# Performance work log

Measured on AMD Instinct MI355X. Metric: run time of the kernel, lower is better.

Reference implementation:

```python
import jax, jax.numpy as jnp
import numpy as np

N = 4096
D = 256          # hidden_dim
H = 8            # num_heads
HD = D // H      # head_dim
EPS = 1e-5
SCALE = D ** -0.5  # note: full hidden_dim, as in the torch code


def setup_inputs() -> dict:
    key = jax.random.key(0)
    ks = jax.random.split(key, 12)
    # binary-ish adjacency mask in [0,1); zeros/near-zeros act like masked entries
    A = (jax.random.uniform(ks[0], (N, N)) < 0.01).astype(jnp.float32)
    h = jax.random.normal(ks[1], (N, D), dtype=jnp.float32)
    s = D ** -0.5
    Wq = jax.random.normal(ks[2], (D, D), dtype=jnp.float32) * s
    Wk = jax.random.normal(ks[3], (D, D), dtype=jnp.float32) * s
    Wv = jax.random.normal(ks[4], (D, D), dtype=jnp.float32) * s
    Wo = jax.random.normal(ks[5], (D, D), dtype=jnp.float32) * s
    g1 = jnp.ones((D,), jnp.float32)
    b1 = jnp.zeros((D,), jnp.float32)
    g2 = jnp.ones((D,), jnp.float32)
    b2 = jnp.zeros((D,), jnp.float32)
    W1 = jax.random.normal(ks[6], (2 * D, D), dtype=jnp.float32) * s
    W2 = jax.random.normal(ks[7], (D, 2 * D), dtype=jnp.float32) * (2 * D) ** -0.5
    return {"A": A, "h": h, "Wq": Wq, "Wk": Wk, "Wv": Wv, "Wo": Wo,
            "g1": g1, "b1": b1, "g2": g2, "b2": b2, "W1": W1, "W2": W2}


def _batchnorm(x, g, b):
    # training-mode BatchNorm1d over node/batch dim, biased variance
    m = x.mean(axis=0)
    v = x.var(axis=0)
    return (x - m) * jax.lax.rsqrt(v + EPS) * g + b


def _mha(A, h, Wq, Wk, Wv, Wo):
    # torch reshape(N, head_dim, num_heads): head index is the fastest axis
    q = (h @ Wq.T).reshape(N, HD, H) * SCALE   # [N, hd, H]
    k = (h @ Wk.T).reshape(N, HD, H)
    v = (h @ Wv.T).reshape(N, HD, H)
    scores = jnp.einsum('ndh,mdh->hnm', q, k)  # [H, N, N]
    attn = jax.nn.softmax(A[None, :, :] * scores, axis=2)
    out = jnp.einsum('hnm,mdh->ndh', attn, v)  # [N, hd, H]
    return out.reshape(N, D) @ Wo.T


def reference(A, h, Wq, Wk, Wv, Wo, g1, b1, g2, b2, W1, W2):
    h1 = h
    h = _mha(A, h, Wq, Wk, Wv, Wo)
    h = h + h1                       # residual
    h = _batchnorm(h, g1, b1)
    h2 = h
    h = jax.nn.relu(h @ W1.T) @ W2.T  # FFN (no bias)
    h = h2 + h                       # residual
    h = _batchnorm(h, g2, b2)
    return h
```

## Files before the change

kernel.cpp:

```cpp
#include <hip/hip_runtime.h>
#include <math.h>

#define NN 4096
#define DIM 256
#define NHEAD 8
#define HDIM 32
#define DFF 512
#define CAP 128
#define EPS_BN 1e-5f
#define QSCALE 0.0625f
#define MB (1u << 20)

typedef __attribute__((ext_vector_type(8))) short short8;
typedef __attribute__((ext_vector_type(4))) float f32x4;

__device__ inline ushort f2bf(float x) {
    unsigned u = __builtin_bit_cast(unsigned, x);
    unsigned r = u + 0x7FFF + ((u >> 16) & 1);
    return (ushort)(r >> 16);
}
__device__ inline float bf2f(ushort u) {
    return __builtin_bit_cast(float, (unsigned)u << 16);
}
__device__ inline float bflo(unsigned u) { return __builtin_bit_cast(float, u << 16); }
__device__ inline float bfhi(unsigned u) { return __builtin_bit_cast(float, u & 0xFFFF0000u); }

__global__ __launch_bounds__(256) void convert_bf(
    const float* __restrict__ s0, const float* __restrict__ s1,
    const float* __restrict__ s2, const float* __restrict__ s3,
    const float* __restrict__ s4, const float* __restrict__ s5,
    const float* __restrict__ s6,
    ushort* d0, ushort* d1, ushort* d2, ushort* d3,
    ushort* d4, ushort* d5, ushort* d6)
{
    int b = blockIdx.x, tid = threadIdx.x;
    if (b >= 608 && b < 640) {
        int off = b - 608;
        int row = off * 8 + (tid >> 5), t = tid & 31;
        int hh = t >> 2, dd0 = (t & 3) * 8;
        const float* src = s4 + (size_t)row * 256 + hh;
        ushort tmp[8];
        #pragma unroll
        for (int i = 0; i < 8; ++i) tmp[i] = f2bf(src[(size_t)(dd0 + i) * 8]);
        uint4 u;
        u.x = (unsigned)tmp[0] | ((unsigned)tmp[1] << 16);
        u.y = (unsigned)tmp[2] | ((unsigned)tmp[3] << 16);
        u.z = (unsigned)tmp[4] | ((unsigned)tmp[5] << 16);
        u.w = (unsigned)tmp[6] | ((unsigned)tmp[7] << 16);
        *(uint4*)(d4 + (size_t)row * 256 + hh * 32 + dd0) = u;
        return;
    }
    const float* s; ushort* d; int off;
    if      (b < 512) { s = s0; d = d0; off = b; }
    else if (b < 544) { s = s1; d = d1; off = b - 512; }
    else if (b < 576) { s = s2; d = d2; off = b - 544; }
    else if (b < 608) { s = s3; d = d3; off = b - 576; }
    else if (b < 704) { s = s5; d = d5; off = b - 640; }
    else              { s = s6; d = d6; off = b - 704; }
    size_t base = (size_t)off * 2048 + (size_t)tid * 8;
    float4 f0 = *(const float4*)(s + base);
    float4 f1 = *(const float4*)(s + base + 4);
    uint4 u;
    u.x = (unsigned)f2bf(f0.x) | ((unsigned)f2bf(f0.y) << 16);
    u.y = (unsigned)f2bf(f0.z) | ((unsigned)f2bf(f0.w) << 16);
    u.z = (unsigned)f2bf(f1.x) | ((unsigned)f2bf(f1.y) << 16);
    u.w = (unsigned)f2bf(f1.z) | ((unsigned)f2bf(f1.w) << 16);
    *(uint4*)(d + base) = u;
}

#define LDP 88
#define TSTRIDE 74
__global__ __launch_bounds__(256) void qkv_ascan(
    const ushort* __restrict__ Ah, const ushort* __restrict__ B,
    ushort* __restrict__ qh, ushort* __restrict__ kvh,
    float* __restrict__ vpart,
    const float* __restrict__ Araw, unsigned* __restrict__ packed,
    int* __restrict__ cnt)
{
    __shared__ ushort As[64][LDP];
    __shared__ ushort Bs[64][LDP];
    __shared__ float sRedS[8][64];
    int b = blockIdx.x, tid = threadIdx.x;

    if (b >= 768) {
        int* scan = (int*)&As[0][0];
        int n = b - 768;
        const float* row = Araw + (size_t)n * NN;
        float4 vals[4];
        int c = 0;
        #pragma unroll
        for (int i = 0; i < 4; ++i) {
            vals[i] = *(const float4*)(row + i * 1024 + tid * 4);
            c += (vals[i].x != 0.f) + (vals[i].y != 0.f)
               + (vals[i].z != 0.f) + (vals[i].w != 0.f);
        }
        scan[tid] = c;
        __syncthreads();
        for (int off = 1; off < 256; off <<= 1) {
            int t = (tid >= off) ? scan[tid - off] : 0;
            __syncthreads();
            scan[tid] += t;
            __syncthreads();
        }
        int pos = scan[tid] - c;
        int total = scan[255];
        #pragma unroll
        for (int i = 0; i < 4; ++i) {
            int cb = i * 1024 + tid * 4;
            float4 v = vals[i];
            if (v.x != 0.f && pos < CAP) { packed[n*CAP+pos] = ((unsigned)f2bf(v.x) << 16) | (unsigned)cb;       ++pos; }
            if (v.y != 0.f && pos < CAP) { packed[n*CAP+pos] = ((unsigned)f2bf(v.y) << 16) | (unsigned)(cb + 1); ++pos; }
            if (v.z != 0.f && pos < CAP) { packed[n*CAP+pos] = ((unsigned)f2bf(v.z) << 16) | (unsigned)(cb + 2); ++pos; }
            if (v.w != 0.f && pos < CAP) { packed[n*CAP+pos] = ((unsigned)f2bf(v.w) << 16) | (unsigned)(cb + 3); ++pos; }
        }
        if (tid == 0) cnt[n] = min(total, CAP);
        return;
    }

    int lane = tid & 63, w = tid >> 6;
    int wm = (w >> 1) * 32, wn = (w & 1) * 32;
    int xcd = b & 7, pos = b >> 3;
    int by = xcd * 8 + pos / 12;
    int bx = pos % 12;
    int m0 = by * 64, n0 = bx * 64;
    int l15 = lane & 15, lk = lane >> 4;
    int srow = tid >> 3;
    int scol = (tid & 7) * 8;

    f32x4 acc[2][2] = {};
    for (int k0 = 0; k0 < DIM; k0 += 64) {
        const ushort* Bg = B + (size_t)(n0 + srow) * DIM + scol + k0;
        uint4 gb0 = *(const uint4*)Bg;
        uint4 gb1 = *(const uint4*)(Bg + (size_t)32 * DIM);
        const ushort* Ag = Ah + (size_t)(m0 + srow) * DIM + scol + k0;
        uint4 ga0 = *(const uint4*)Ag;
        uint4 ga1 = *(const uint4*)(Ag + (size_t)32 * DIM);
        __syncthreads();
        *(uint4*)&As[srow][scol]      = ga0;
        *(uint4*)&As[srow + 32][scol] = ga1;
        *(uint4*)&Bs[srow][scol]      = gb0;
        *(uint4*)&Bs[srow + 32][scol] = gb1;
        __syncthreads();
        #pragma unroll
        for (int ks = 0; ks < 2; ++ks) {
            int kc = ks * 32 + lk * 8;
            short8 a0 = *(const short8*)&As[wm      + l15][kc];
            short8 a1 = *(const short8*)&As[wm + 16 + l15][kc];
            short8 b0 = *(const short8*)&Bs[wn      + l15][kc];
            short8 b1 = *(const short8*)&Bs[wn + 16 + l15][kc];
            acc[0][0] = __builtin_amdgcn_mfma_f32_16x16x32_bf16(a0, b0, acc[0][0], 0, 0, 0);
            acc[0][1] = __builtin_amdgcn_mfma_f32_16x16x32_bf16(a0, b1, acc[0][1], 0, 0, 0);
            acc[1][0] = __builtin_amdgcn_mfma_f32_16x16x32_bf16(a1, b0, acc[1][0], 0, 0, 0);
            acc[1][1] = __builtin_amdgcn_mfma_f32_16x16x32_bf16(a1, b1, acc[1][1], 0, 0, 0);
        }
    }
    ushort* sT = &As[0][0];
    int seg = n0 >> 8, ddBase = (n0 & 255) >> 3;
    float sp[2] = {0.f, 0.f};
    __syncthreads();
    #pragma unroll
    for (int mt = 0; mt < 2; ++mt)
        #pragma unroll
        for (int nt = 0; nt < 2; ++nt) {
            int col_l = wn + nt * 16 + l15;
            #pragma unroll
            for (int i = 0; i < 4; ++i) {
                int row_l = wm + mt * 16 + lk * 4 + i;
                float v = acc[mt][nt][i];
                if (seg == 0) v *= QSCALE;
                sT[row_l * TSTRIDE + col_l] = f2bf(v);
                sp[nt] += v;
            }
        }
    __syncthreads();
    for (int c = tid; c < 512; c += 256) {
        int rl = c & 63, hh = c >> 6;
        const ushort* tp = sT + rl * TSTRIDE + hh;
        uint4 pk;
        pk.x = (unsigned)tp[0]  | ((unsigned)tp[8]  << 16);
        pk.y = (unsigned)tp[16] | ((unsigned)tp[24] << 16);
        pk.z = (unsigned)tp[32] | ((unsigned)tp[40] << 16);
        pk.w = (unsigned)tp[48] | ((unsigned)tp[56] << 16);
        int row = m0 + rl;
        if (seg == 0)
            *(uint4*)(qh + ((size_t)hh * NN + row) * HDIM + ddBase) = pk;
        else
            *(uint4*)(kvh + ((size_t)hh * NN + row) * 64 +
                      ((seg == 2) ? 32 : 0) + ddBase) = pk;
    }
    if (seg == 2) {
        int slot = ((wm >> 5) << 2) | lk;
        sRedS[slot][wn + l15]      = sp[0];
        sRedS[slot][wn + 16 + l15] = sp[1];
        __syncthreads();
        if (tid < 64) {
            float ss = 0.f;
            #pragma unroll
            for (int r = 0; r < 8; ++r) ss += sRedS[r][tid];
            vpart[(size_t)by * 256 + (n0 & 255) + tid] = ss;
        }
    }
}

__global__ __launch_bounds__(256) void gemm_bf(
    const void* __restrict__ Aptr, const ushort* __restrict__ B,
    const float* __restrict__ scA, const float* __restrict__ shA,
    const float* __restrict__ resid,
    const float* yres, const float* __restrict__ scR, const float* __restrict__ shR,
    float* Cf, ushort* __restrict__ Cb,
    float* __restrict__ bnps, float* __restrict__ bnpq,
    int M, int Nn, int K, int aMode, int storeMode, int relu, int bnstat)
{
    __shared__ ushort As[64][LDP];
    __shared__ ushort Bs[64][LDP];
    __shared__ float sRedS[8][64];
    __shared__ float sRedQ[8][64];
    int tid = threadIdx.x;
    int lane = tid & 63, w = tid >> 6;
    int wm = (w >> 1) * 32, wn = (w & 1) * 32;
    int nbx = gridDim.x, nbyq = gridDim.y >> 3;
    int orig = blockIdx.y * nbx + blockIdx.x;
    int xcd = orig & 7, pos = orig >> 3;
    int by = xcd * nbyq + pos / nbx;
    int bx = pos % nbx;
    int m0 = by * 64, n0 = bx * 64;
    int l15 = lane & 15, lk = lane >> 4;
    int srow = tid >> 3;
    int scol = (tid & 7) * 8;

    f32x4 acc[2][2] = {};
    for (int k0 = 0; k0 < K; k0 += 64) {
        uint4 ga0, ga1, gb0, gb1;
        const ushort* Bg = B + (size_t)(n0 + srow) * K + scol + k0;
        gb0 = *(const uint4*)Bg;
        gb1 = *(const uint4*)(Bg + (size_t)32 * K);
        if (aMode == 0) {
            const ushort* Ag = (const ushort*)Aptr + (size_t)(m0 + srow) * K + scol + k0;
            ga0 = *(const uint4*)Ag;
            ga1 = *(const uint4*)(Ag + (size_t)32 * K);
        } else if (aMode == 2) {
            int c0 = k0 + scol;
            int hh = c0 >> 5, dd = c0 & 31;
            const ushort* Ag = (const ushort*)Aptr +
                ((size_t)hh * NN + m0 + srow) * HDIM + dd;
            ga0 = *(const uint4*)Ag;
            ga1 = *(const uint4*)(Ag + (size_t)32 * HDIM);
        } else {
            const float* Af = (const float*)Aptr + (size_t)(m0 + srow) * K + scol + k0;
            float4 sc0 = *(const float4*)(scA + k0 + scol);
            float4 sc1 = *(const float4*)(scA + k0 + scol + 4);
            float4 sh0 = *(const float4*)(shA + k0 + scol);
            float4 sh1 = *(const float4*)(shA + k0 + scol + 4);
            float4 a0 = *(const float4*)Af;
            float4 a1 = *(const float4*)(Af + 4);
            float4 b0 = *(const float4*)(Af + (size_t)32 * K);
            float4 b1 = *(const float4*)(Af + (size_t)32 * K + 4);
            ga0.x = (unsigned)f2bf(a0.x*sc0.x+sh0.x) | ((unsigned)f2bf(a0.y*sc0.y+sh0.y) << 16);
            ga0.y = (unsigned)f2bf(a0.z*sc0.z+sh0.z) | ((unsigned)f2bf(a0.w*sc0.w+sh0.w) << 16);
            ga0.z = (unsigned)f2bf(a1.x*sc1.x+sh1.x) | ((unsigned)f2bf(a1.y*sc1.y+sh1.y) << 16);
            ga0.w = (unsigned)f2bf(a1.z*sc1.z+sh1.z) | ((unsigned)f2bf(a1.w*sc1.w+sh1.w) << 16);
            ga1.x = (unsigned)f2bf(b0.x*sc0.x+sh0.x) | ((unsigned)f2bf(b0.y*sc0.y+sh0.y) << 16);
            ga1.y = (unsigned)f2bf(b0.z*sc0.z+sh0.z) | ((unsigned)f2bf(b0.w*sc0.w+sh0.w) << 16);
            ga1.z = (unsigned)f2bf(b1.x*sc1.x+sh1.x) | ((unsigned)f2bf(b1.y*sc1.y+sh1.y) << 16);
            ga1.w = (unsigned)f2bf(b1.z*sc1.z+sh1.z) | ((unsigned)f2bf(b1.w*sc1.w+sh1.w) << 16);
        }
        __syncthreads();
        *(uint4*)&As[srow][scol]      = ga0;
        *(uint4*)&As[srow + 32][scol] = ga1;
        *(uint4*)&Bs[srow][scol]      = gb0;
        *(uint4*)&Bs[srow + 32][scol] = gb1;
        __syncthreads();
        #pragma unroll
        for (int ks = 0; ks < 2; ++ks) {
            int kc = ks * 32 + lk * 8;
            short8 a0 = *(const short8*)&As[wm      + l15][kc];
            short8 a1 = *(const short8*)&As[wm + 16 + l15][kc];
            short8 b0 = *(const short8*)&Bs[wn      + l15][kc];
            short8 b1 = *(const short8*)&Bs[wn + 16 + l15][kc];
            acc[0][0] = __builtin_amdgcn_mfma_f32_16x16x32_bf16(a0, b0, acc[0][0], 0, 0, 0);
            acc[0][1] = __builtin_amdgcn_mfma_f32_16x16x32_bf16(a0, b1, acc[0][1], 0, 0, 0);
            acc[1][0] = __builtin_amdgcn_mfma_f32_16x16x32_bf16(a1, b0, acc[1][0], 0, 0, 0);
            acc[1][1] = __builtin_amdgcn_mfma_f32_16x16x32_bf16(a1, b1, acc[1][1], 0, 0, 0);
        }
    }

    float sp[2] = {0.f, 0.f}, qp[2] = {0.f, 0.f};
    #pragma unroll
    for (int mt = 0; mt < 2; ++mt) {
        #pragma unroll
        for (int nt = 0; nt < 2; ++nt) {
            int col = n0 + wn + nt * 16 + l15;
            #pragma unroll
            for (int i = 0; i < 4; ++i) {
                int row = m0 + wm + mt * 16 + lk * 4 + i;
                float v = acc[mt][nt][i];
                if (storeMode == 0) {
                    if (resid) v += resid[(size_t)row * Nn + col];
                    Cf[(size_t)row * Nn + col] = v;
                } else if (storeMode == 1) {
                    if (relu) v = fmaxf(v, 0.f);
                    Cb[(size_t)row * Nn + col] = f2bf(v);
                } else {
                    v += yres[(size_t)row * Nn + col] * scR[col] + shR[col];
                    Cf[(size_t)row * Nn + col] = v;
                }
                if (bnstat) { sp[nt] += v; qp[nt] += v * v; }
            }
        }
    }
    if (bnstat) {
        int slot = ((wm >> 5) << 2) | lk;
        sRedS[slot][wn + l15]      = sp[0];
        sRedQ[slot][wn + l15]      = qp[0];
        sRedS[slot][wn + 16 + l15] = sp[1];
        sRedQ[slot][wn + 16 + l15] = qp[1];
        __syncthreads();
        if (tid < 64) {
            float ss = 0.f, qq = 0.f;
            #pragma unroll
            for (int r = 0; r < 8; ++r) { ss += sRedS[r][tid]; qq += sRedQ[r][tid]; }
            bnps[(size_t)by * DIM + n0 + tid] = ss;
            bnpq[(size_t)by * DIM + n0 + tid] = qq;
        }
    }
}

__global__ __launch_bounds__(256) void vsum_final(
    const float* __restrict__ vpart, float* __restrict__ vsumh)
{
    int c = threadIdx.x;
    float s = 0.f;
    #pragma unroll 8
    for (int b = 0; b < 64; ++b) s += vpart[(size_t)b * 256 + c];
    vsumh[(c & 7) * HDIM + (c >> 3)] = s;
}

__global__ __launch_bounds__(1024) void colreduce_final2(
    const float* __restrict__ ps, const float* __restrict__ pq,
    const float* __restrict__ g, const float* __restrict__ bsh,
    float* __restrict__ scale, float* __restrict__ shift)
{
    __shared__ float rs_[4][256], rq_[4][256];
    int t = threadIdx.x;
    int c = t & 255, qd = t >> 8;
    float s = 0.f, q = 0.f;
    for (int b = qd; b < 64; b += 4) {
        s += ps[b * DIM + c];
        q += pq[b * DIM + c];
    }
    rs_[qd][c] = s; rq_[qd][c] = q;
    __syncthreads();
    if (qd == 0) {
        s = rs_[0][c] + rs_[1][c] + rs_[2][c] + rs_[3][c];
        q = rq_[0][c] + rq_[1][c] + rq_[2][c] + rq_[3][c];
        float m = s * (1.f / NN);
        float var = q * (1.f / NN) - m * m;
        float rstd = rsqrtf(var + EPS_BN);
        float sc = rstd * g[c];
        scale[c] = sc;
        shift[c] = bsh[c] - m * sc;
    }
}

__global__ __launch_bounds__(256) void bn_apply_fin(
    const float* __restrict__ x, const float* __restrict__ scale,
    const float* __restrict__ shift, float* __restrict__ out)
{
    int tid = threadIdx.x;
    size_t i = (size_t)blockIdx.x * 1024 + (size_t)tid * 4;
    int c = (tid * 4) & 255;
    float4 v = *(const float4*)(x + i);
    float4 sc = *(const float4*)(scale + c);
    float4 sh = *(const float4*)(shift + c);
    float4 r;
    r.x = v.x * sc.x + sh.x;
    r.y = v.y * sc.y + sh.y;
    r.z = v.z * sc.z + sh.z;
    r.w = v.w * sc.w + sh.w;
    *(float4*)(out + i) = r;
}

__global__ __launch_bounds__(256) void attn3(
    const ushort* __restrict__ qh, const ushort* __restrict__ kvh,
    const float* __restrict__ vsumh,
    const unsigned* __restrict__ packed, const int* __restrict__ cnt,
    ushort* __restrict__ outh)
{
    __shared__ float    sQ[8][32];
    __shared__ unsigned sPk[8][CAP];
    __shared__ float    sS[8][CAP];
    __shared__ float    sRd[8];

    int tid = threadIdx.x, b = blockIdx.x;
    int hH = b & 7, rg = b >> 3;
    int r = tid >> 5, l = tid & 31;
    int n = rg * 8 + r;
    int nnz = cnt[n];

    sQ[r][l] = bf2f(qh[((size_t)hH * NN + n) * HDIM + l]);
    for (int j = l; j < nnz; j += 32) sPk[r][j] = packed[n * CAP + j];
    __syncthreads();

    float4 qreg[8];
    #pragma unroll
    for (int t = 0; t < 8; ++t) qreg[t] = ((const float4*)sQ[r])[t];
    float lsum = 0.0f;
    for (int j = l; j < nnz; j += 32) {
        unsigned pk = sPk[r][j];
        int m = pk & 0xFFFF;
        float a = bfhi(pk);
        const uint4* kp = (const uint4*)(kvh + ((size_t)hH * NN + m) * 64);
        uint4 k0 = kp[0], k1 = kp[1], k2 = kp[2], k3 = kp[3];
        float s =
            bflo(k0.x)*qreg[0].x + bfhi(k0.x)*qreg[0].y +
            bflo(k0.y)*qreg[0].z + bfhi(k0.y)*qreg[0].w +
            bflo(k0.z)*qreg[1].x + bfhi(k0.z)*qreg[1].y +
            bflo(k0.w)*qreg[1].z + bfhi(k0.w)*qreg[1].w +
            bflo(k1.x)*qreg[2].x + bfhi(k1.x)*qreg[2].y +
            bflo(k1.y)*qreg[2].z + bfhi(k1.y)*qreg[2].w +
            bflo(k1.z)*qreg[3].x + bfhi(k1.z)*qreg[3].y +
            bflo(k1.w)*qreg[3].z + bfhi(k1.w)*qreg[3].w +
            bflo(k2.x)*qreg[4].x + bfhi(k2.x)*qreg[4].y +
            bflo(k2.y)*qreg[4].z + bfhi(k2.y)*qreg[4].w +
            bflo(k2.z)*qreg[5].x + bfhi(k2.z)*qreg[5].y +
            bflo(k2.w)*qreg[5].z + bfhi(k2.w)*qreg[5].w +
            bflo(k3.x)*qreg[6].x + bfhi(k3.x)*qreg[6].y +
            bflo(k3.y)*qreg[6].z + bfhi(k3.y)*qreg[6].w +
            bflo(k3.z)*qreg[7].x + bfhi(k3.z)*qreg[7].y +
            bflo(k3.w)*qreg[7].z + bfhi(k3.w)*qreg[7].w;
        s *= a;
        float ww = __expf(s);
        sS[r][j] = ww - 1.0f;
        lsum += ww;
    }
    #pragma unroll
    for (int o = 16; o > 0; o >>= 1) lsum += __shfl_xor(lsum, o, 32);
    if (l == 0) sRd[r] = 1.0f / (lsum + (float)(NN - nnz));
    __syncthreads();

    int jsub = l >> 3, dq = l & 7;
    const ushort* vbase = kvh + (size_t)hH * NN * 64 + 32 + dq * 4;
    float a0 = 0.f, a1 = 0.f, a2 = 0.f, a3 = 0.f;
    for (int j = jsub; j < nnz; j += 4) {
        float ww = sS[r][j];
        int m = sPk[r][j] & 0xFFFF;
        uint2 vv = *(const uint2*)(vbase + (size_t)m * 64);
        a0 += ww * bflo(vv.x); a1 += ww * bfhi(vv.x);
        a2 += ww * bflo(vv.y); a3 += ww * bfhi(vv.y);
    }
    #pragma unroll
    for (int o = 8; o < 32; o <<= 1) {
        a0 += __shfl_xor(a0, o, 32);
        a1 += __shfl_xor(a1, o, 32);
        a2 += __shfl_xor(a2, o, 32);
        a3 += __shfl_xor(a3, o, 32);
    }
    if (jsub == 0) {
        float rd = sRd[r];
        int d0 = dq * 4;
        const float* vs = vsumh + hH * HDIM + d0;
        float r0 = (a0 + vs[0]) * rd;
        float r1 = (a1 + vs[1]) * rd;
        float r2 = (a2 + vs[2]) * rd;
        float r3 = (a3 + vs[3]) * rd;
        uint2 st;
        st.x = (unsigned)f2bf(r0) | ((unsigned)f2bf(r1) << 16);
        st.y = (unsigned)f2bf(r2) | ((unsigned)f2bf(r3) << 16);
        *(uint2*)(outh + ((size_t)hH * NN + n) * HDIM + d0) = st;
    }
}

extern "C" void kernel_launch(void* const* d_in, const int* in_sizes, int n_in,
                              void* d_out, int out_size, void* d_ws, size_t ws_size,
                              hipStream_t stream)
{
    const float* A  = (const float*)d_in[0];
    const float* h  = (const float*)d_in[1];
    const float* Wq = (const float*)d_in[2];
    const float* Wk = (const float*)d_in[3];
    const float* Wv = (const float*)d_in[4];
    const float* Wo = (const float*)d_in[5];
    const float* g1 = (const float*)d_in[6];
    const float* b1 = (const float*)d_in[7];
    const float* g2 = (const float*)d_in[8];
    const float* b2 = (const float*)d_in[9];
    const float* W1 = (const float*)d_in[10];
    const float* W2 = (const float*)d_in[11];
    float* out = (float*)d_out;
    char* w = (char*)d_ws;

    unsigned* packed = (unsigned*)(w);
    int*    nzcnt  = (int*)(w + 2 * MB);
    ushort* h_bf   = (ushort*)(w + 3 * MB);
    ushort* wqkv   = (ushort*)(w + 5 * MB);
    ushort* wo_b   = (ushort*)(w + 5 * MB + 384 * 1024);
    ushort* w1_b   = (ushort*)(w + 5 * MB + 512 * 1024);
    ushort* w2_b   = (ushort*)(w + 5 * MB + 768 * 1024);
    ushort* qh_bf  = (ushort*)(w + 6 * MB);
    ushort* kvh    = (ushort*)(w + 8 * MB);
    ushort* ao_hb  = (ushort*)(w + 12 * MB);
    float*  y      = (float*)(w + 14 * MB);
    ushort* t_bf   = (ushort*)(w + 18 * MB);
    float*  vpart  = (float*)(w + 22 * MB);
    float*  bnps   = (float*)(w + 23 * MB);
    float*  bnpq   = (float*)(w + 23 * MB + 64 * 1024);
    float*  scale1 = (float*)(w + 24 * MB);
    float*  shift1 = scale1 + 256;
    float*  scale2 = scale1 + 512;
    float*  shift2 = scale1 + 768;
    float*  vsumh  = scale1 + 1024;

    dim3 blk(256);

    convert_bf<<<768, blk, 0, stream>>>(h, Wq, Wk, Wv, Wo, W1, W2,
        h_bf, wqkv, wqkv + 65536, wqkv + 131072, wo_b, w1_b, w2_b);
    qkv_ascan<<<4864, blk, 0, stream>>>(h_bf, wqkv, qh_bf, kvh, vpart,
                                        A, packed, nzcnt);
    vsum_final<<<1, blk, 0, stream>>>(vpart, vsumh);
    attn3<<<NN, blk, 0, stream>>>(qh_bf, kvh, vsumh, packed, nzcnt, ao_hb);
    gemm_bf<<<dim3(4, 64), blk, 0, stream>>>(ao_hb, wo_b,
        nullptr, nullptr, h, nullptr, nullptr, nullptr,
        y, nullptr, bnps, bnpq, NN, DIM, DIM, 2, 0, 0, 1);
    colreduce_final2<<<1, dim3(1024), 0, stream>>>(bnps, bnpq, g1, b1, scale1, shift1);
    gemm_bf<<<dim3(8, 64), blk, 0, stream>>>(y, w1_b,
        scale1, shift1, nullptr, nullptr, nullptr, nullptr,
        nullptr, t_bf, nullptr, nullptr, NN, DFF, DIM, 1, 1, 1, 0);
    gemm_bf<<<dim3(4, 64), blk, 0, stream>>>(t_bf, w2_b,
        nullptr, nullptr, nullptr, y, scale1, shift1,
        y, nullptr, bnps, bnpq, NN, DIM, DFF, 0, 3, 0, 1);
    colreduce_final2<<<1, dim3(1024), 0, stream>>>(bnps, bnpq, g2, b2, scale2, shift2);
    bn_apply_fin<<<1024, blk, 0, stream>>>(y, scale2, shift2, out);
}
```

Before: 94.94 us.

## Fold reduction finalizers into producer kernels via last-block atomics; convert h inline

Removes the separate vsum_final and colreduce_final2 launches by having the last-finishing block (detected with an atomic counter and threadfence) do the final column reduction inside qkv_ascan and the BN-stat gemm_bf calls. The fp32 input h is now converted to bf16 while being loaded into the QKV GEMM instead of in a separate pass, so convert_w handles only the weights and resets the counters. This cuts three kernel launches and one global round trip for h_bf. In exchange, each GEMM tile now converts its A operand itself, and one block per kernel does a serial 64-row reduction at the tail.

```diff
diff --git a/kernel.cpp b/kernel.cpp
--- a/kernel.cpp
+++ b/kernel.cpp
@@ -25,20 +25,21 @@
 __device__ inline float bflo(unsigned u) { return __builtin_bit_cast(float, u << 16); }
 __device__ inline float bfhi(unsigned u) { return __builtin_bit_cast(float, u & 0xFFFF0000u); }
 
-__global__ __launch_bounds__(256) void convert_bf(
-    const float* __restrict__ s0, const float* __restrict__ s1,
-    const float* __restrict__ s2, const float* __restrict__ s3,
-    const float* __restrict__ s4, const float* __restrict__ s5,
-    const float* __restrict__ s6,
-    ushort* d0, ushort* d1, ushort* d2, ushort* d3,
-    ushort* d4, ushort* d5, ushort* d6)
+__global__ __launch_bounds__(256) void convert_w(
+    const float* __restrict__ Wq, const float* __restrict__ Wk,
+    const float* __restrict__ Wv, const float* __restrict__ Wo,
+    const float* __restrict__ W1, const float* __restrict__ W2,
+    ushort* __restrict__ wqkv, ushort* __restrict__ wo_b,
+    ushort* __restrict__ w1_b, ushort* __restrict__ w2_b,
+    int* __restrict__ cnts)
 {
     int b = blockIdx.x, tid = threadIdx.x;
-    if (b >= 608 && b < 640) {
-        int off = b - 608;
+    if (b == 0 && tid < 8) cnts[tid] = 0;
+    if (b >= 96 && b < 128) {
+        int off = b - 96;
         int row = off * 8 + (tid >> 5), t = tid & 31;
         int hh = t >> 2, dd0 = (t & 3) * 8;
-        const float* src = s4 + (size_t)row * 256 + hh;
+        const float* src = Wo + (size_t)row * 256 + hh;
         ushort tmp[8];
         #pragma unroll
         for (int i = 0; i < 8; ++i) tmp[i] = f2bf(src[(size_t)(dd0 + i) * 8]);
@@ -47,16 +48,15 @@
         u.y = (unsigned)tmp[2] | ((unsigned)tmp[3] << 16);
         u.z = (unsigned)tmp[4] | ((unsigned)tmp[5] << 16);
         u.w = (unsigned)tmp[6] | ((unsigned)tmp[7] << 16);
-        *(uint4*)(d4 + (size_t)row * 256 + hh * 32 + dd0) = u;
+        *(uint4*)(wo_b + (size_t)row * 256 + hh * 32 + dd0) = u;
         return;
     }
     const float* s; ushort* d; int off;
-    if      (b < 512) { s = s0; d = d0; off = b; }
-    else if (b < 544) { s = s1; d = d1; off = b - 512; }
-    else if (b < 576) { s = s2; d = d2; off = b - 544; }
-    else if (b < 608) { s = s3; d = d3; off = b - 576; }
-    else if (b < 704) { s = s5; d = d5; off = b - 640; }
-    else              { s = s6; d = d6; off = b - 704; }
+    if      (b < 32)  { s = Wq; d = wqkv;          off = b; }
+    else if (b < 64)  { s = Wk; d = wqkv + 65536;  off = b - 32; }
+    else if (b < 96)  { s = Wv; d = wqkv + 131072; off = b - 64; }
+    else if (b < 192) { s = W1; d = w1_b;          off = b - 128; }
+    else              { s = W2; d = w2_b;          off = b - 192; }
     size_t base = (size_t)off * 2048 + (size_t)tid * 8;
     float4 f0 = *(const float4*)(s + base);
     float4 f1 = *(const float4*)(s + base + 4);
@@ -71,15 +71,16 @@
 #define LDP 88
 #define TSTRIDE 74
 __global__ __launch_bounds__(256) void qkv_ascan(
-    const ushort* __restrict__ Ah, const ushort* __restrict__ B,
+    const float* __restrict__ hF, const ushort* __restrict__ B,
     ushort* __restrict__ qh, ushort* __restrict__ kvh,
-    float* __restrict__ vpart,
+    float* __restrict__ vpart, float* __restrict__ vsumh,
     const float* __restrict__ Araw, unsigned* __restrict__ packed,
-    int* __restrict__ cnt)
+    int* __restrict__ cnt, int* __restrict__ cntV)
 {
     __shared__ ushort As[64][LDP];
     __shared__ ushort Bs[64][LDP];
     __shared__ float sRedS[8][64];
+    __shared__ int lastF;
     int b = blockIdx.x, tid = threadIdx.x;
 
     if (b >= 768) {
@@ -132,9 +133,20 @@
         const ushort* Bg = B + (size_t)(n0 + srow) * DIM + scol + k0;
         uint4 gb0 = *(const uint4*)Bg;
         uint4 gb1 = *(const uint4*)(Bg + (size_t)32 * DIM);
-        const ushort* Ag = Ah + (size_t)(m0 + srow) * DIM + scol + k0;
-        uint4 ga0 = *(const uint4*)Ag;
-        uint4 ga1 = *(const uint4*)(Ag + (size_t)32 * DIM);
+        const float* Af = hF + (size_t)(m0 + srow) * DIM + scol + k0;
+        float4 a0 = *(const float4*)Af;
+        float4 a1 = *(const float4*)(Af + 4);
+        float4 c0 = *(const float4*)(Af + (size_t)32 * DIM);
+        float4 c1 = *(const float4*)(Af + (size_t)32 * DIM + 4);
+        uint4 ga0, ga1;
+        ga0.x = (unsigned)f2bf(a0.x) | ((unsigned)f2bf(a0.y) << 16);
+        ga0.y = (unsigned)f2bf(a0.z) | ((unsigned)f2bf(a0.w) << 16);
+        ga0.z = (unsigned)f2bf(a1.x) | ((unsigned)f2bf(a1.y) << 16);
+        ga0.w = (unsigned)f2bf(a1.z) | ((unsigned)f2bf(a1.w) << 16);
+        ga1.x = (unsigned)f2bf(c0.x) | ((unsigned)f2bf(c0.y) << 16);
+        ga1.y = (unsigned)f2bf(c0.z) | ((unsigned)f2bf(c0.w) << 16);
+        ga1.z = (unsigned)f2bf(c1.x) | ((unsigned)f2bf(c1.y) << 16);
+        ga1.w = (unsigned)f2bf(c1.z) | ((unsigned)f2bf(c1.w) << 16);
         __syncthreads();
         *(uint4*)&As[srow][scol]      = ga0;
         *(uint4*)&As[srow + 32][scol] = ga1;
@@ -144,14 +156,14 @@
         #pragma unroll
         for (int ks = 0; ks < 2; ++ks) {
             int kc = ks * 32 + lk * 8;
-            short8 a0 = *(const short8*)&As[wm      + l15][kc];
-            short8 a1 = *(const short8*)&As[wm + 16 + l15][kc];
-            short8 b0 = *(const short8*)&Bs[wn      + l15][kc];
-            short8 b1 = *(const short8*)&Bs[wn + 16 + l15][kc];
-            acc[0][0] = __builtin_amdgcn_mfma_f32_16x16x32_bf16(a0, b0, acc[0][0], 0, 0, 0);
-            acc[0][1] = __builtin_amdgcn_mfma_f32_16x16x32_bf16(a0, b1, acc[0][1], 0, 0, 0);
-            acc[1][0] = __builtin_amdgcn_mfma_f32_16x16x32_bf16(a1, b0, acc[1][0], 0, 0, 0);
-            acc[1][1] = __builtin_amdgcn_mfma_f32_16x16x32_bf16(a1, b1, acc[1][1], 0, 0, 0);
+            short8 a0s = *(const short8*)&As[wm      + l15][kc];
+            short8 a1s = *(const short8*)&As[wm + 16 + l15][kc];
+            short8 b0s = *(const short8*)&Bs[wn      + l15][kc];
+            short8 b1s = *(const short8*)&Bs[wn + 16 + l15][kc];
+            acc[0][0] = __builtin_amdgcn_mfma_f32_16x16x32_bf16(a0s, b0s, acc[0][0], 0, 0, 0);
+            acc[0][1] = __builtin_amdgcn_mfma_f32_16x16x32_bf16(a0s, b1s, acc[0][1], 0, 0, 0);
+            acc[1][0] = __builtin_amdgcn_mfma_f32_16x16x32_bf16(a1s, b0s, acc[1][0], 0, 0, 0);
+            acc[1][1] = __builtin_amdgcn_mfma_f32_16x16x32_bf16(a1s, b1s, acc[1][1], 0, 0, 0);
         }
     }
     ushort* sT = &As[0][0];
@@ -199,6 +211,17 @@
             for (int r = 0; r < 8; ++r) ss += sRedS[r][tid];
             vpart[(size_t)by * 256 + (n0 & 255) + tid] = ss;
         }
+        __threadfence();
+        if (tid == 0) lastF = (atomicAdd(cntV, 1) == 255);
+        __syncthreads();
+        if (lastF) {
+            __threadfence();
+            int c = tid;
+            float s = 0.f;
+            #pragma unroll 8
+            for (int bb = 0; bb < 64; ++bb) s += vpart[(size_t)bb * 256 + c];
+            vsumh[(c & 7) * HDIM + (c >> 3)] = s;
+        }
     }
 }
 
@@ -209,12 +232,16 @@
     const float* yres, const float* __restrict__ scR, const float* __restrict__ shR,
     float* Cf, ushort* __restrict__ Cb,
     float* __restrict__ bnps, float* __restrict__ bnpq,
+    int* __restrict__ lastCnt, const float* __restrict__ g,
+    const float* __restrict__ bsh, float* __restrict__ scaleOut,
+    float* __restrict__ shiftOut,
     int M, int Nn, int K, int aMode, int storeMode, int relu, int bnstat)
 {
     __shared__ ushort As[64][LDP];
     __shared__ ushort Bs[64][LDP];
     __shared__ float sRedS[8][64];
     __shared__ float sRedQ[8][64];
+    __shared__ int lastF;
     int tid = threadIdx.x;
     int lane = tid & 63, w = tid >> 6;
     int wm = (w >> 1) * 32, wn = (w & 1) * 32;
@@ -322,43 +349,26 @@
             bnps[(size_t)by * DIM + n0 + tid] = ss;
             bnpq[(size_t)by * DIM + n0 + tid] = qq;
         }
-    }
-}
-
-__global__ __launch_bounds__(256) void vsum_final(
-    const float* __restrict__ vpart, float* __restrict__ vsumh)
-{
-    int c = threadIdx.x;
-    float s = 0.f;
-    #pragma unroll 8
-    for (int b = 0; b < 64; ++b) s += vpart[(size_t)b * 256 + c];
-    vsumh[(c & 7) * HDIM + (c >> 3)] = s;
-}
-
-__global__ __launch_bounds__(1024) void colreduce_final2(
-    const float* __restrict__ ps, const float* __restrict__ pq,
-    const float* __restrict__ g, const float* __restrict__ bsh,
-    float* __restrict__ scale, float* __restrict__ shift)
-{
-    __shared__ float rs_[4][256], rq_[4][256];
-    int t = threadIdx.x;
-    int c = t & 255, qd = t >> 8;
-    float s = 0.f, q = 0.f;
-    for (int b = qd; b < 64; b += 4) {
-        s += ps[b * DIM + c];
-        q += pq[b * DIM + c];
-    }
-    rs_[qd][c] = s; rq_[qd][c] = q;
-    __syncthreads();
-    if (qd == 0) {
-        s = rs_[0][c] + rs_[1][c] + rs_[2][c] + rs_[3][c];
-        q = rq_[0][c] + rq_[1][c] + rq_[2][c] + rq_[3][c];
-        float m = s * (1.f / NN);
-        float var = q * (1.f / NN) - m * m;
-        float rstd = rsqrtf(var + EPS_BN);
-        float sc = rstd * g[c];
-        scale[c] = sc;
-        shift[c] = bsh[c] - m * sc;
+        __threadfence();
+        if (tid == 0)
+            lastF = (atomicAdd(lastCnt, 1) == (int)(gridDim.x * gridDim.y) - 1);
+        __syncthreads();
+        if (lastF) {
+            __threadfence();
+            int c = tid;
+            float s = 0.f, q = 0.f;
+            #pragma unroll 4
+            for (int bb = 0; bb < 64; ++bb) {
+                s += bnps[(size_t)bb * DIM + c];
+                q += bnpq[(size_t)bb * DIM + c];
+            }
+            float m = s * (1.f / NN);
+            float var = q * (1.f / NN) - m * m;
+            float rstd = rsqrtf(var + EPS_BN);
+            float sc = rstd * g[c];
+            scaleOut[c] = sc;
+            shiftOut[c] = bsh[c] - m * sc;
+        }
     }
 }
 
@@ -491,7 +501,6 @@
 
     unsigned* packed = (unsigned*)(w);
     int*    nzcnt  = (int*)(w + 2 * MB);
-    ushort* h_bf   = (ushort*)(w + 3 * MB);
     ushort* wqkv   = (ushort*)(w + 5 * MB);
     ushort* wo_b   = (ushort*)(w + 5 * MB + 384 * 1024);
     ushort* w1_b   = (ushort*)(w + 5 * MB + 512 * 1024);
@@ -502,32 +511,35 @@
     float*  y      = (float*)(w + 14 * MB);
     ushort* t_bf   = (ushort*)(w + 18 * MB);
     float*  vpart  = (float*)(w + 22 * MB);
-    float*  bnps   = (float*)(w + 23 * MB);
-    float*  bnpq   = (float*)(w + 23 * MB + 64 * 1024);
+    float*  bnps1  = (float*)(w + 23 * MB);
+    float*  bnpq1  = (float*)(w + 23 * MB + 64 * 1024);
+    float*  bnps2  = (float*)(w + 23 * MB + 128 * 1024);
+    float*  bnpq2  = (float*)(w + 23 * MB + 192 * 1024);
     float*  scale1 = (float*)(w + 24 * MB);
     float*  shift1 = scale1 + 256;
     float*  scale2 = scale1 + 512;
     float*  shift2 = scale1 + 768;
     float*  vsumh  = scale1 + 1024;
+    int*    cnts   = (int*)(w + 25 * MB);
 
     dim3 blk(256);
 
-    convert_bf<<<768, blk, 0, stream>>>(h, Wq, Wk, Wv, Wo, W1, W2,
-        h_bf, wqkv, wqkv + 65536, wqkv + 131072, wo_b, w1_b, w2_b);
-    qkv_ascan<<<4864, blk, 0, stream>>>(h_bf, wqkv, qh_bf, kvh, vpart,
-                                        A, packed, nzcnt);
-    vsum_final<<<1, blk, 0, stream>>>(vpart, vsumh);
+    convert_w<<<256, blk, 0, stream>>>(Wq, Wk, Wv, Wo, W1, W2,
+        wqkv, wo_b, w1_b, w2_b, cnts);
+    qkv_ascan<<<4864, blk, 0, stream>>>(h, wqkv, qh_bf, kvh, vpart, vsumh,
+                                        A, packed, nzcnt, cnts + 0);
     attn3<<<NN, blk, 0, stream>>>(qh_bf, kvh, vsumh, packed, nzcnt, ao_hb);
     gemm_bf<<<dim3(4, 64), blk, 0, stream>>>(ao_hb, wo_b,
         nullptr, nullptr, h, nullptr, nullptr, nullptr,
-        y, nullptr, bnps, bnpq, NN, DIM, DIM, 2, 0, 0, 1);
-    colreduce_final2<<<1, dim3(1024), 0, stream>>>(bnps, bnpq, g1, b1, scale1, shift1);
+        y, nullptr, bnps1, bnpq1, cnts + 1, g1, b1, scale1, shift1,
+        NN, DIM, DIM, 2, 0, 0, 1);
     gemm_bf<<<dim3(8, 64), blk, 0, stream>>>(y, w1_b,
         scale1, shift1, nullptr, nullptr, nullptr, nullptr,
-        nullptr, t_bf, nullptr, nullptr, NN, DFF, DIM, 1, 1, 1, 0);
+        nullptr, t_bf, nullptr, nullptr, nullptr, nullptr, nullptr,
+        nullptr, nullptr, NN, DFF, DIM, 1, 1, 1, 0);
     gemm_bf<<<dim3(4, 64), blk, 0, stream>>>(t_bf, w2_b,
         nullptr, nullptr, nullptr, y, scale1, shift1,
-        y, nullptr, bnps, bnpq, NN, DIM, DFF, 0, 3, 0, 1);
-    colreduce_final2<<<1, dim3(1024), 0, stream>>>(bnps, bnpq, g2, b2, scale2, shift2);
+        y, nullptr, bnps2, bnpq2, cnts + 2, g2, b2, scale2, shift2,
+        NN, DIM, DFF, 0, 3, 0, 1);
     bn_apply_fin<<<1024, blk, 0, stream>>>(y, scale2, shift2, out);
 }
```

Measured after the change: 164.1 us. 1.73x slower.

## Fuse attention score and value accumulation into one pass per neighbor

Applied to the files above, without the earlier changes.

The sparse attention kernel now loads K and V for each neighbor in the same pass and accumulates exp-weighted V into 32 per-lane registers. This replaces the separate second loop that re-gathered V rows and read scores back from shared memory. A transposed shared-memory reduction across lanes then produces the output, in two batches to bound LDS use. The cost is higher register pressure (32 accumulators) and a larger LDS reduction with extra barriers. Q is also kept packed as bf16 and unpacked on the fly.

```diff
diff --git a/kernel.cpp b/kernel.cpp
--- a/kernel.cpp
+++ b/kernel.cpp
@@ -200,6 +200,16 @@
             vpart[(size_t)by * 256 + (n0 & 255) + tid] = ss;
         }
     }
+}
+
+__global__ __launch_bounds__(256) void vsum_final(
+    const float* __restrict__ vpart, float* __restrict__ vsumh)
+{
+    int c = threadIdx.x;
+    float s = 0.f;
+    #pragma unroll 8
+    for (int b = 0; b < 64; ++b) s += vpart[(size_t)b * 256 + c];
+    vsumh[(c & 7) * HDIM + (c >> 3)] = s;
 }
 
 __global__ __launch_bounds__(256) void gemm_bf(
@@ -325,16 +335,6 @@
     }
 }
 
-__global__ __launch_bounds__(256) void vsum_final(
-    const float* __restrict__ vpart, float* __restrict__ vsumh)
-{
-    int c = threadIdx.x;
-    float s = 0.f;
-    #pragma unroll 8
-    for (int b = 0; b < 64; ++b) s += vpart[(size_t)b * 256 + c];
-    vsumh[(c & 7) * HDIM + (c >> 3)] = s;
-}
-
 __global__ __launch_bounds__(1024) void colreduce_final2(
     const float* __restrict__ ps, const float* __restrict__ pq,
     const float* __restrict__ g, const float* __restrict__ bsh,
@@ -380,16 +380,16 @@
     *(float4*)(out + i) = r;
 }
 
-__global__ __launch_bounds__(256) void attn3(
+__global__ __launch_bounds__(256) void attn4(
     const ushort* __restrict__ qh, const ushort* __restrict__ kvh,
     const float* __restrict__ vsumh,
     const unsigned* __restrict__ packed, const int* __restrict__ cnt,
     ushort* __restrict__ outh)
 {
-    __shared__ float    sQ[8][32];
+    __shared__ unsigned sQp[8][16];
     __shared__ unsigned sPk[8][CAP];
-    __shared__ float    sS[8][CAP];
     __shared__ float    sRd[8];
+    __shared__ float    sRed[4][32][33];
 
     int tid = threadIdx.x, b = blockIdx.x;
     int hH = b & 7, rg = b >> 3;
@@ -397,76 +397,82 @@
     int n = rg * 8 + r;
     int nnz = cnt[n];
 
-    sQ[r][l] = bf2f(qh[((size_t)hH * NN + n) * HDIM + l]);
+    if (l < 16)
+        sQp[r][l] = ((const unsigned*)(qh + ((size_t)hH * NN + n) * HDIM))[l];
     for (int j = l; j < nnz; j += 32) sPk[r][j] = packed[n * CAP + j];
     __syncthreads();
 
-    float4 qreg[8];
+    float acc[32];
     #pragma unroll
-    for (int t = 0; t < 8; ++t) qreg[t] = ((const float4*)sQ[r])[t];
-    float lsum = 0.0f;
+    for (int i = 0; i < 32; ++i) acc[i] = 0.f;
+    float lsum = 0.f;
+
     for (int j = l; j < nnz; j += 32) {
         unsigned pk = sPk[r][j];
         int m = pk & 0xFFFF;
         float a = bfhi(pk);
         const uint4* kp = (const uint4*)(kvh + ((size_t)hH * NN + m) * 64);
         uint4 k0 = kp[0], k1 = kp[1], k2 = kp[2], k3 = kp[3];
+        uint4 v0 = kp[4], v1 = kp[5], v2 = kp[6], v3 = kp[7];
+        const unsigned* q = sQp[r];
         float s =
-            bflo(k0.x)*qreg[0].x + bfhi(k0.x)*qreg[0].y +
-            bflo(k0.y)*qreg[0].z + bfhi(k0.y)*qreg[0].w +
-            bflo(k0.z)*qreg[1].x + bfhi(k0.z)*qreg[1].y +
-            bflo(k0.w)*qreg[1].z + bfhi(k0.w)*qreg[1].w +
-            bflo(k1.x)*qreg[2].x + bfhi(k1.x)*qreg[2].y +
-            bflo(k1.y)*qreg[2].z + bfhi(k1.y)*qreg[2].w +
-            bflo(k1.z)*qreg[3].x + bfhi(k1.z)*qreg[3].y +
-            bflo(k1.w)*qreg[3].z + bfhi(k1.w)*qreg[3].w +
-            bflo(k2.x)*qreg[4].x + bfhi(k2.x)*qreg[4].y +
-            bflo(k2.y)*qreg[4].z + bfhi(k2.y)*qreg[4].w +
-            bflo(k2.z)*qreg[5].x + bfhi(k2.z)*qreg[5].y +
-            bflo(k2.w)*qreg[5].z + bfhi(k2.w)*qreg[5].w +
-            bflo(k3.x)*qreg[6].x + bfhi(k3.x)*qreg[6].y +
-            bflo(k3.y)*qreg[6].z + bfhi(k3.y)*qreg[6].w +
-            bflo(k3.z)*qreg[7].x + bfhi(k3.z)*qreg[7].y +
-            bflo(k3.w)*qreg[7].z + bfhi(k3.w)*qreg[7].w;
+            bflo(k0.x)*bflo(q[0])  + bfhi(k0.x)*bfhi(q[0])  +
+            bflo(k0.y)*bflo(q[1])  + bfhi(k0.y)*bfhi(q[1])  +
+            bflo(k0.z)*bflo(q[2])  + bfhi(k0.z)*bfhi(q[2])  +
+            bflo(k0.w)*bflo(q[3])  + bfhi(k0.w)*bfhi(q[3])  +
+            bflo(k1.x)*bflo(q[4])  + bfhi(k1.x)*bfhi(q[4])  +
+            bflo(k1.y)*bflo(q[5])  + bfhi(k1.y)*bfhi(q[5])  +
+            bflo(k1.z)*bflo(q[6])  + bfhi(k1.z)*bfhi(q[6])  +
+            bflo(k1.w)*bflo(q[7])  + bfhi(k1.w)*bfhi(q[7])  +
+            bflo(k2.x)*bflo(q[8])  + bfhi(k2.x)*bfhi(q[8])  +
+            bflo(k2.y)*bflo(q[9])  + bfhi(k2.y)*bfhi(q[9])  +
+            bflo(k2.z)*bflo(q[10]) + bfhi(k2.z)*bfhi(q[10]) +
+            bflo(k2.w)*bflo(q[11]) + bfhi(k2.w)*bfhi(q[11]) +
+            bflo(k3.x)*bflo(q[12]) + bfhi(k3.x)*bfhi(q[12]) +
+            bflo(k3.y)*bflo(q[13]) + bfhi(k3.y)*bfhi(q[13]) +
+            bflo(k3.z)*bflo(q[14]) + bfhi(k3.z)*bfhi(q[14]) +
+            bflo(k3.w)*bflo(q[15]) + bfhi(k3.w)*bfhi(q[15]);
         s *= a;
         float ww = __expf(s);
-        sS[r][j] = ww - 1.0f;
         lsum += ww;
-    }
+        float wm1 = ww - 1.0f;
+        acc[0]  += wm1 * bflo(v0.x); acc[1]  += wm1 * bfhi(v0.x);
+        acc[2]  += wm1 * bflo(v0.y); acc[3]  += wm1 * bfhi(v0.y);
+        acc[4]  += wm1 * bflo(v0.z); acc[5]  += wm1 * bfhi(v0.z);
+        acc[6]  += wm1 * bflo(v0.w); acc[7]  += wm1 * bfhi(v0.w);
+        acc[8]  += wm1 * bflo(v1.x); acc[9]  += wm1 * bfhi(v1.x);
+        acc[10] += wm1 * bflo(v1.y); acc[11] += wm1 * bfhi(v1.y);
+        acc[12] += wm1 * bflo(v1.z); acc[13] += wm1 * bfhi(v1.z);
+        acc[14] += wm1 * bflo(v1.w); acc[15] += wm1 * bfhi(v1.w);
+        acc[16] += wm1 * bflo(v2.x); acc[17] += wm1 * bfhi(v2.x);
+        acc[18] += wm1 * bflo(v2.y); acc[19] += wm1 * bfhi(v2.y);
+        acc[20] += wm1 * bflo(v2.z); acc[21] += wm1 * bfhi(v2.z);
+        acc[22] += wm1 * bflo(v2.w); acc[23] += wm1 * bfhi(v2.w);
+        acc[24] += wm1 * bflo(v3.x); acc[25] += wm1 * bfhi(v3.x);
+        acc[26] += wm1 * bflo(v3.y); acc[27] += wm1 * bfhi(v3.y);
+        acc[28] += wm1 * bflo(v3.z); acc[29] += wm1 * bfhi(v3.z);
+        acc[30] += wm1 * bflo(v3.w); acc[31] += wm1 * bfhi(v3.w);
+    }
+
     #pragma unroll
     for (int o = 16; o > 0; o >>= 1) lsum += __shfl_xor(lsum, o, 32);
     if (l == 0) sRd[r] = 1.0f / (lsum + (float)(NN - nnz));
-    __syncthreads();
-
-    int jsub = l >> 3, dq = l & 7;
-    const ushort* vbase = kvh + (size_t)hH * NN * 64 + 32 + dq * 4;
-    float a0 = 0.f, a1 = 0.f, a2 = 0.f, a3 = 0.f;
-    for (int j = jsub; j < nnz; j += 4) {
-        float ww = sS[r][j];
-        int m = sPk[r][j] & 0xFFFF;
-        uint2 vv = *(const uint2*)(vbase + (size_t)m * 64);
-        a0 += ww * bflo(vv.x); a1 += ww * bfhi(vv.x);
-        a2 += ww * bflo(vv.y); a3 += ww * bfhi(vv.y);
-    }
+
     #pragma unroll
-    for (int o = 8; o < 32; o <<= 1) {
-        a0 += __shfl_xor(a0, o, 32);
-        a1 += __shfl_xor(a1, o, 32);
-        a2 += __shfl_xor(a2, o, 32);
-        a3 += __shfl_xor(a3, o, 32);
-    }
-    if (jsub == 0) {
-        float rd = sRd[r];
-        int d0 = dq * 4;
-        const float* vs = vsumh + hH * HDIM + d0;
-        float r0 = (a0 + vs[0]) * rd;
-        float r1 = (a1 + vs[1]) * rd;
-        float r2 = (a2 + vs[2]) * rd;
-        float r3 = (a3 + vs[3]) * rd;
-        uint2 st;
-        st.x = (unsigned)f2bf(r0) | ((unsigned)f2bf(r1) << 16);
-        st.y = (unsigned)f2bf(r2) | ((unsigned)f2bf(r3) << 16);
-        *(uint2*)(outh + ((size_t)hH * NN + n) * HDIM + d0) = st;
+    for (int batch = 0; batch < 2; ++batch) {
+        __syncthreads();
+        if ((r >> 2) == batch) {
+            #pragma unroll
+            for (int i = 0; i < 32; ++i) sRed[r & 3][l][i] = acc[i];
+        }
+        __syncthreads();
+        if ((r >> 2) == batch) {
+            float o = 0.f;
+            #pragma unroll
+            for (int src = 0; src < 32; ++src) o += sRed[r & 3][src][l];
+            float res = (o + vsumh[hH * HDIM + l]) * sRd[r];
+            outh[((size_t)hH * NN + n) * HDIM + l] = f2bf(res);
+        }
     }
 }
 
@@ -517,7 +523,7 @@
     qkv_ascan<<<4864, blk, 0, stream>>>(h_bf, wqkv, qh_bf, kvh, vpart,
                                         A, packed, nzcnt);
     vsum_final<<<1, blk, 0, stream>>>(vpart, vsumh);
-    attn3<<<NN, blk, 0, stream>>>(qh_bf, kvh, vsumh, packed, nzcnt, ao_hb);
+    attn4<<<NN, blk, 0, stream>>>(qh_bf, kvh, vsumh, packed, nzcnt, ao_hb);
     gemm_bf<<<dim3(4, 64), blk, 0, stream>>>(ao_hb, wo_b,
         nullptr, nullptr, h, nullptr, nullptr, nullptr,
         y, nullptr, bnps, bnpq, NN, DIM, DIM, 2, 0, 0, 1);
```

Result: slower. 103.1 us (+8.6%).
